# Kernel tuning notes

Measured on AMD Instinct MI355X. Metric: run time of the kernel, lower is better.

## Reference

```python
import jax, jax.numpy as jnp
import numpy as np
from jax import lax

N = 100000
IN_C, HID, OUT_C = 512, 256, 128
K_STEPS = 10
ALPHA = 0.1
RES_ALPHA = 1.0
LN_EPS = 1e-5


def layer_norm(h, g, b):
    mu = jnp.mean(h, axis=-1, keepdims=True)
    var = jnp.mean(jnp.square(h - mu), axis=-1, keepdims=True)
    return (h - mu) * lax.rsqrt(var + LN_EPS) * g + b


def appnp(h, src, dst):
    # add self loops
    loop = jnp.arange(N, dtype=src.dtype)
    s = jnp.concatenate([src, loop])
    d = jnp.concatenate([dst, loop])
    ew = jnp.ones(s.shape[0], h.dtype)
    deg = jax.ops.segment_sum(ew, d, num_segments=N)
    dis = jnp.where(deg > 0, lax.rsqrt(jnp.maximum(deg, 1e-12)), 0.0)
    norm = dis[s] * ew * dis[d]  # [E+N]
    h0 = h
    def step(carry, _):
        msg = norm[:, None] * carry[s]                      # gather [E+N, C]
        agg = jax.ops.segment_sum(msg, d, num_segments=N)    # scatter-add
        return (1.0 - ALPHA) * agg + ALPHA * h0, None
    h, _ = lax.scan(step, h, None, length=K_STEPS)
    return h


def setup_inputs() -> dict:
    key = jax.random.key(0)
    ks = jax.random.split(key, 12)
    def lin(k, fan_in, fan_out):
        bound = 1.0 / np.sqrt(fan_in)
        kw, kb = jax.random.split(k)
        W = jax.random.uniform(kw, (fan_in, fan_out), jnp.float32, -bound, bound)
        b = jax.random.uniform(kb, (fan_out,), jnp.float32, -bound, bound)
        return W, b
    x = jax.random.normal(ks[0], (N, IN_C), jnp.float32)
    edge_index = jax.random.randint(ks[1], (2, 1600000), 0, N, jnp.int32)
    W_in, b_in = lin(ks[2], IN_C, HID)
    W1, b1 = lin(ks[3], HID, HID)
    W2, b2 = lin(ks[4], HID, HID)
    W_out, b_out = lin(ks[5], HID, OUT_C)
    g1 = jnp.ones(HID); be1 = jnp.zeros(HID)
    g2 = jnp.ones(HID); be2 = jnp.zeros(HID)
    return {"x": x, "edge_index": edge_index,
            "W_in": W_in, "b_in": b_in,
            "W1": W1, "b1": b1, "g1": g1, "be1": be1,
            "W2": W2, "b2": b2, "g2": g2, "be2": be2,
            "W_out": W_out, "b_out": b_out}


def reference(x, edge_index, W_in, b_in, W1, b1, g1, be1, W2, b2, g2, be2, W_out, b_out):
    # MLP with residual blocks (eval mode: no dropout)
    h = x @ W_in + b_in
    for (W, b, g, be) in ((W1, b1, g1, be1), (W2, b2, g2, be2)):
        identity = h
        h = layer_norm(h @ W + b, g, be)
        h = RES_ALPHA * h + (1.0 - RES_ALPHA) * identity
        h = jax.nn.relu(h)
    h = h @ W_out + b_out
    # APPNP propagation
    return appnp(h, edge_index[0], edge_index[1])
```

## Files before the change

kernel.cpp:

```cpp
#include <hip/hip_runtime.h>

typedef unsigned short u16;
typedef unsigned long long u64;
typedef __attribute__((ext_vector_type(8))) short bfrag;
typedef __attribute__((ext_vector_type(4))) float f32x4;

__device__ inline float b2f(u16 u) {
    union { unsigned int i; float f; } v; v.i = ((unsigned int)u) << 16; return v.f;
}
__device__ inline u16 f2b(float f) {
    union { float f; unsigned int u; } v; v.f = f;
    unsigned int r = v.u + 0x7fffu + ((v.u >> 16) & 1u);
    return (u16)(r >> 16);
}
__device__ inline float ldF(const void* p, size_t i, bool bf) {
    return bf ? b2f(((const u16*)p)[i]) : ((const float*)p)[i];
}
__device__ inline void gload_lds16(const void* g, void* l) {
    __builtin_amdgcn_global_load_lds((const __attribute__((address_space(1))) unsigned int*)g,
                                     (__attribute__((address_space(3))) unsigned int*)l, 16, 0, 0);
}

__global__ void detect_k(const unsigned int* __restrict__ g1w, int* flag) {
    if (blockIdx.x == 0 && threadIdx.x == 0)
        *flag = (g1w[0] == 0x3F803F80u) ? 1 : 0;
}

__global__ void wt_k(const void* __restrict__ W, u16* __restrict__ Wt, int K, int NC,
                     const int* __restrict__ flagp) {
    int i = blockIdx.x * 256 + threadIdx.x;
    if (i >= K * NC) return;
    int k = i / NC, nn = i - k * NC;
    u16 v = (*flagp) ? ((const u16*)W)[i] : f2b(((const float*)W)[i]);
    Wt[(size_t)nn * K + k] = v;
}

template<int K, bool OUT_BF16, bool A_DUAL>
__global__ __launch_bounds__(256) void gemm_bt(const void* __restrict__ Ain, const u16* __restrict__ Bt,
                                               const void* __restrict__ bias, void* __restrict__ C,
                                               int M, int NC, const int* __restrict__ flagp) {
    const int BM = 128, BN = 128, BK = 32;
    __shared__ u16 As[2][BM * BK];
    __shared__ u16 Bs[2][BN * BK];
    const bool bf = (*flagp != 0);
    int nt = NC / BN;

    int nwg = gridDim.x, bid = blockIdx.x;
    int qc = nwg >> 3, rc = nwg & 7;
    int xcd = bid & 7, off = bid >> 3;
    int swz = (xcd < rc ? xcd * (qc + 1) : rc * (qc + 1) + (xcd - rc) * qc) + off;
    int m0 = (swz / nt) * BM;
    int n0 = (swz % nt) * BN;

    int t = threadIdx.x;
    int lane = t & 63, wave = t >> 6;
    int wm = (wave >> 1) * 64, wn = (wave & 1) * 64;

    f32x4 acc[4][4];
#pragma unroll
    for (int i = 0; i < 4; i++)
#pragma unroll
        for (int j = 0; j < 4; j++) acc[i][j] = (f32x4){0.f, 0.f, 0.f, 0.f};

    auto stage = [&](int bufi, int kk) {
#pragma unroll
        for (int q = 0; q < 2; ++q) {
            int idx = q * 256 + t;
            int row = idx >> 2;
            int cb  = (idx & 3) * 16;
            int ra = m0 + row; ra = ra < M ? ra : M - 1;
            const char* gb = (const char*)Bt + ((size_t)(n0 + row) * K) * 2 + kk * 2 + cb;
            char* la = (char*)&As[bufi][0] + q * 4096 + wave * 1024;
            char* lb = (char*)&Bs[bufi][0] + q * 4096 + wave * 1024;
            if (!A_DUAL || bf) {
                const char* ga = (const char*)Ain + ((size_t)ra * K) * 2 + kk * 2 + cb;
                gload_lds16(ga, la);
            } else {
                const float* gaf = (const float*)Ain + (size_t)ra * K + kk + (cb >> 1);
                float4 f0 = *(const float4*)gaf;
                float4 f1 = *(const float4*)(gaf + 4);
                ushort4 o0, o1;
                o0.x = f2b(f0.x); o0.y = f2b(f0.y); o0.z = f2b(f0.z); o0.w = f2b(f0.w);
                o1.x = f2b(f1.x); o1.y = f2b(f1.y); o1.z = f2b(f1.z); o1.w = f2b(f1.w);
                *(ushort4*)(la + (size_t)lane * 16)     = o0;
                *(ushort4*)(la + (size_t)lane * 16 + 8) = o1;
            }
            gload_lds16(gb, lb);
        }
    };

    stage(0, 0);
    __syncthreads();
    int cur = 0;
    int r16 = lane & 15, q8 = (lane >> 4) * 8;
    for (int k0 = 0; k0 < K; k0 += BK) {
        if (k0 + BK < K) stage(cur ^ 1, k0 + BK);
        bfrag a[4], b[4];
#pragma unroll
        for (int i = 0; i < 4; i++) a[i] = *(const bfrag*)&As[cur][(wm + i * 16 + r16) * BK + q8];
#pragma unroll
        for (int j = 0; j < 4; j++) b[j] = *(const bfrag*)&Bs[cur][(wn + j * 16 + r16) * BK + q8];
#pragma unroll
        for (int i = 0; i < 4; i++)
#pragma unroll
            for (int j = 0; j < 4; j++)
                acc[i][j] = __builtin_amdgcn_mfma_f32_16x16x32_bf16(a[i], b[j], acc[i][j], 0, 0, 0);
        __syncthreads();
        cur ^= 1;
    }

    int q4 = (lane >> 4) * 4;
#pragma unroll
    for (int j = 0; j < 4; j++) {
        int cg = n0 + wn + j * 16 + r16;
        float bvv = ldF(bias, cg, bf);
#pragma unroll
        for (int i = 0; i < 4; i++) {
#pragma unroll
            for (int rr = 0; rr < 4; rr++) {
                int rg = m0 + wm + i * 16 + q4 + rr;
                if (rg < M) {
                    float v = acc[i][j][rr] + bvv;
                    if (OUT_BF16) ((u16*)C)[(size_t)rg * NC + cg] = f2b(v);
                    else          ((float*)C)[(size_t)rg * NC + cg] = v;
                }
            }
        }
    }
}

__global__ __launch_bounds__(256) void ln_relu_k(const u16* __restrict__ T, const void* __restrict__ g,
                                                 const void* __restrict__ be, u16* __restrict__ out,
                                                 int M, const int* __restrict__ flagp) {
    const bool bf = (*flagp != 0);
    int wave = threadIdx.x >> 6, lane = threadIdx.x & 63;
    int row = blockIdx.x * 4 + wave;
    if (row >= M) return;
    const ushort4 xq = *(const ushort4*)(T + (size_t)row * 256 + lane * 4);
    float x0 = b2f(xq.x), x1 = b2f(xq.y), x2 = b2f(xq.z), x3 = b2f(xq.w);
    float s = x0 + x1 + x2 + x3;
    for (int o = 32; o > 0; o >>= 1) s += __shfl_xor(s, o);
    float mu = s * (1.0f / 256.0f);
    float d0 = x0 - mu, d1 = x1 - mu, d2 = x2 - mu, d3 = x3 - mu;
    float q = d0 * d0 + d1 * d1 + d2 * d2 + d3 * d3;
    for (int o = 32; o > 0; o >>= 1) q += __shfl_xor(q, o);
    float rs = rsqrtf(q * (1.0f / 256.0f) + 1e-5f);
    int c0 = lane * 4;
    float y0 = fmaxf(d0 * rs * ldF(g, c0 + 0, bf) + ldF(be, c0 + 0, bf), 0.f);
    float y1 = fmaxf(d1 * rs * ldF(g, c0 + 1, bf) + ldF(be, c0 + 1, bf), 0.f);
    float y2 = fmaxf(d2 * rs * ldF(g, c0 + 2, bf) + ldF(be, c0 + 2, bf), 0.f);
    float y3 = fmaxf(d3 * rs * ldF(g, c0 + 3, bf) + ldF(be, c0 + 3, bf), 0.f);
    ushort4 o4; o4.x = f2b(y0); o4.y = f2b(y1); o4.z = f2b(y2); o4.w = f2b(y3);
    *(ushort4*)(out + (size_t)row * 256 + c0) = o4;
}

__global__ void deg_count(const int* __restrict__ dst, int* deg, int E) {
    int i = blockIdx.x * 256 + threadIdx.x;
    if (i < E) atomicAdd(&deg[dst[i]], 1);
}
__global__ void dis_k(const int* __restrict__ deg, float* dis, int n) {
    int i = blockIdx.x * 256 + threadIdx.x;
    if (i < n) dis[i] = rsqrtf((float)(deg[i] + 1));
}

__global__ void scan_block(const int* __restrict__ deg, int* rowptr, int* bsum, int n) {
    __shared__ int sh[256];
    int t = threadIdx.x, i = blockIdx.x * 256 + t;
    int v = (i < n) ? deg[i] + 1 : 0;
    sh[t] = v; __syncthreads();
    for (int o = 1; o < 256; o <<= 1) {
        int x = (t >= o) ? sh[t - o] : 0;
        __syncthreads();
        sh[t] += x;
        __syncthreads();
    }
    if (i < n) rowptr[i] = sh[t] - v;
    if (t == 255) bsum[blockIdx.x] = sh[t];
}
__global__ void scan_sums(int* bsum, int nb) {
    __shared__ int sh[512];
    int t = threadIdx.x;
    int v = (t < nb) ? bsum[t] : 0;
    sh[t] = v; __syncthreads();
    for (int o = 1; o < 512; o <<= 1) {
        int x = (t >= o) ? sh[t - o] : 0;
        __syncthreads();
        sh[t] += x;
        __syncthreads();
    }
    if (t < nb) bsum[t] = sh[t] - v;
}
__global__ void scan_add(int* rowptr, const int* __restrict__ bsum, int n, int total) {
    int i = blockIdx.x * 256 + threadIdx.x;
    if (i < n) rowptr[i] += bsum[blockIdx.x];
    if (i == 0) rowptr[n] = total;
}
__global__ void fill_k(const int* __restrict__ src, const int* __restrict__ dst,
                       const int* __restrict__ rowptr, int* cursor, const float* __restrict__ dis,
                       int2* __restrict__ epack, int E, int n) {
    int i = blockIdx.x * 256 + threadIdx.x;
    if (i >= E + n) return;
    int s, d;
    if (i < E) { s = src[i]; d = dst[i]; }
    else       { s = d = i - E; }
    int p = rowptr[d] + atomicAdd(&cursor[d], 1);
    float wv = dis[s] * dis[d];
    u64 e = ((u64)__float_as_uint(wv) << 32) | (unsigned int)s;
    __builtin_nontemporal_store(e, (u64*)&epack[p]);
}

__global__ __launch_bounds__(256) void prop_k(const u16* __restrict__ curb, const u16* __restrict__ h0b,
                                              const int* __restrict__ rowptr, const int2* __restrict__ epack,
                                              u16* __restrict__ outB, void* __restrict__ outD,
                                              const int* __restrict__ flagp, int n) {
    int wave = threadIdx.x >> 6, lane = threadIdx.x & 63;
    int node = blockIdx.x * 4 + wave;
    if (node >= n) return;
    int p0 = rowptr[node], p1 = rowptr[node + 1];
    float ax = 0.f, ay = 0.f;
    for (int p = p0; p < p1; p += 64) {
        int cnt = p1 - p; if (cnt > 64) cnt = 64;
        int sj = 0; float wj = 0.f;
        if (lane < cnt) {
            u64 e = __builtin_nontemporal_load((const u64*)(epack + p + lane));
            sj = (int)(unsigned int)e;
            wj = __uint_as_float((unsigned int)(e >> 32));
        }
        int j = 0;
        for (; j + 16 <= cnt; j += 16) {
            float ww[16]; unsigned int v[16];
#pragma unroll
            for (int u = 0; u < 16; ++u) {
                int ss = __shfl(sj, j + u);
                ww[u] = __shfl(wj, j + u);
                v[u] = *(const unsigned int*)(curb + (size_t)ss * 128 + 2 * lane);
            }
#pragma unroll
            for (int u = 0; u < 16; ++u) {
                ax = fmaf(ww[u], b2f((u16)(v[u] & 0xffffu)), ax);
                ay = fmaf(ww[u], b2f((u16)(v[u] >> 16)), ay);
            }
        }
        for (; j < cnt; j += 8) {
            float ww[8]; unsigned int v[8];
#pragma unroll
            for (int u = 0; u < 8; ++u) {
                int jj = j + u;
                bool ok = jj < cnt;
                if (!ok) jj = cnt - 1;
                int ss = __shfl(sj, jj);
                float w2 = __shfl(wj, jj);
                ww[u] = ok ? w2 : 0.f;
                v[u] = *(const unsigned int*)(curb + (size_t)ss * 128 + 2 * lane);
            }
#pragma unroll
            for (int u = 0; u < 8; ++u) {
                ax = fmaf(ww[u], b2f((u16)(v[u] & 0xffffu)), ax);
                ay = fmaf(ww[u], b2f((u16)(v[u] >> 16)), ay);
            }
        }
    }
    unsigned int hp = __builtin_nontemporal_load((const unsigned int*)h0b + (size_t)node * 64 + lane);
    float rx = 0.9f * ax + 0.1f * b2f((u16)(hp & 0xffffu));
    float ry = 0.9f * ay + 0.1f * b2f((u16)(hp >> 16));
    unsigned int pk = ((unsigned int)f2b(ry) << 16) | (unsigned int)f2b(rx);
    if (outB) {
        __builtin_nontemporal_store(pk, (unsigned int*)outB + (size_t)node * 64 + lane);
    } else if (*flagp) {
        __builtin_nontemporal_store(pk, (unsigned int*)outD + (size_t)node * 64 + lane);
    } else {
        u64 o = ((u64)__float_as_uint(ry) << 32) | __float_as_uint(rx);
        __builtin_nontemporal_store(o, (u64*)((float*)outD + (size_t)node * 128 + 2 * lane));
    }
}

extern "C" void kernel_launch(void* const* d_in, const int* in_sizes, int n_in,
                              void* d_out, int out_size, void* d_ws, size_t ws_size,
                              hipStream_t stream) {
    const int N = in_sizes[0] / 512;
    const int E = in_sizes[1] / 2;
    const void* x    = d_in[0];
    const int*  ei   = (const int*)d_in[1];
    const void* Win  = d_in[2];
    const void* bin  = d_in[3];
    const void* W1   = d_in[4];
    const void* b1   = d_in[5];
    const void* g1   = d_in[6];
    const void* be1  = d_in[7];
    const void* W2   = d_in[8];
    const void* b2   = d_in[9];
    const void* g2   = d_in[10];
    const void* be2  = d_in[11];
    const void* Wout = d_in[12];
    const void* bout = d_in[13];
    (void)n_in; (void)out_size; (void)ws_size;

    char* w = (char*)d_ws;
    auto alloc = [&](size_t b) { char* p = w; w += (b + 255) & ~(size_t)255; return p; };
    char*  buf0 = alloc((size_t)N * 512 * 2);
    char*  actAraw = alloc((size_t)N * 256 * 2);
    u16* WtIn  = (u16*)alloc((size_t)512 * 256 * 2);
    u16* Wt1   = (u16*)alloc((size_t)256 * 256 * 2);
    u16* Wt2   = (u16*)alloc((size_t)256 * 256 * 2);
    u16* WtOut = (u16*)alloc((size_t)256 * 128 * 2);
    int*   deg    = (int*)alloc((size_t)N * 4);
    float* dis    = (float*)alloc((size_t)N * 4);
    int*   rowptr = (int*)alloc((size_t)(N + 1) * 4);
    int*   cursor = (int*)alloc((size_t)N * 4);
    int*   bsum   = (int*)alloc(512 * 4);
    int*   flag   = (int*)alloc(256);
    u16*   Tb  = (u16*)buf0;
    u16*   h0b = (u16*)buf0;
    u16*   cA  = (u16*)(buf0 + (size_t)N * 128 * 2);
    u16*   cB  = (u16*)(buf0 + (size_t)N * 128 * 4);
    u16*   actA  = (u16*)actAraw;
    int2*  epack = (int2*)actAraw;

    detect_k<<<1, 64, 0, stream>>>((const unsigned int*)g1, flag);

    wt_k<<<(512 * 256 + 255) / 256, 256, 0, stream>>>(Win,  WtIn,  512, 256, flag);
    wt_k<<<(256 * 256 + 255) / 256, 256, 0, stream>>>(W1,   Wt1,   256, 256, flag);
    wt_k<<<(256 * 256 + 255) / 256, 256, 0, stream>>>(W2,   Wt2,   256, 256, flag);
    wt_k<<<(256 * 128 + 255) / 256, 256, 0, stream>>>(Wout, WtOut, 256, 128, flag);

    int mt = (N + 127) / 128;
    gemm_bt<512, true , true ><<<mt * 2, 256, 0, stream>>>(x,    WtIn,  bin,  actA, N, 256, flag);
    gemm_bt<256, true , false><<<mt * 2, 256, 0, stream>>>(actA, Wt1,   b1,   Tb,   N, 256, flag);
    ln_relu_k<<<(N + 3) / 4, 256, 0, stream>>>(Tb, g1, be1, actA, N, flag);
    gemm_bt<256, true , false><<<mt * 2, 256, 0, stream>>>(actA, Wt2,   b2,   Tb,   N, 256, flag);
    ln_relu_k<<<(N + 3) / 4, 256, 0, stream>>>(Tb, g2, be2, actA, N, flag);
    gemm_bt<256, true , false><<<mt * 1, 256, 0, stream>>>(actA, WtOut, bout, h0b,  N, 128, flag);

    hipMemsetAsync(deg, 0, (size_t)N * 4, stream);
    deg_count<<<(E + 255) / 256, 256, 0, stream>>>(ei + E, deg, E);
    dis_k    <<<(N + 255) / 256, 256, 0, stream>>>(deg, dis, N);
    int nb = (N + 255) / 256;
    scan_block<<<nb, 256, 0, stream>>>(deg, rowptr, bsum, N);
    scan_sums<<<1, 512, 0, stream>>>(bsum, nb);
    scan_add<<<nb, 256, 0, stream>>>(rowptr, bsum, N, E + N);
    hipMemsetAsync(cursor, 0, (size_t)N * 4, stream);
    fill_k<<<(E + N + 255) / 256, 256, 0, stream>>>(ei, ei + E, rowptr, cursor, dis, epack, E, N);

    const u16* cur = h0b;
    for (int it = 0; it < 10; ++it) {
        bool last = (it == 9);
        u16* o = (it & 1) ? cB : cA;
        prop_k<<<(N + 3) / 4, 256, 0, stream>>>(cur, h0b, rowptr, epack,
                                                last ? nullptr : o,
                                                last ? d_out : nullptr, flag, N);
        cur = o;
    }
}
```

Measured before the change: 1.451 ms.

## Overlap fp32 A loads with MFMA and stage GEMM epilogue through LDS

For the fp32-input GEMM, the A tile's global loads are now issued before the MFMAs and converted and written to LDS after them, so load latency overlaps compute instead of stalling the stage. The epilogue writes bf16 results into a swizzled LDS tile and then stores full 16-byte rows, replacing scattered 2-byte global stores. Shared memory is merged into one 32KB buffer reused for the output tile. The cost is extra registers for the prefetched floats and one more barrier per block.

```diff
diff --git a/kernel.cpp b/kernel.cpp
--- a/kernel.cpp
+++ b/kernel.cpp
@@ -35,13 +35,12 @@
     Wt[(size_t)nn * K + k] = v;
 }
 
-template<int K, bool OUT_BF16, bool A_DUAL>
+template<int K, bool A_DUAL>
 __global__ __launch_bounds__(256) void gemm_bt(const void* __restrict__ Ain, const u16* __restrict__ Bt,
-                                               const void* __restrict__ bias, void* __restrict__ C,
+                                               const void* __restrict__ bias, u16* __restrict__ C,
                                                int M, int NC, const int* __restrict__ flagp) {
     const int BM = 128, BN = 128, BK = 32;
-    __shared__ u16 As[2][BM * BK];
-    __shared__ u16 Bs[2][BN * BK];
+    __shared__ u16 sh[16384];
     const bool bf = (*flagp != 0);
     int nt = NC / BN;
 
@@ -62,49 +61,71 @@
 #pragma unroll
         for (int j = 0; j < 4; j++) acc[i][j] = (f32x4){0.f, 0.f, 0.f, 0.f};
 
-    auto stage = [&](int bufi, int kk) {
+    char* shb = (char*)sh;
+    auto ldsA = [&](int bufi) { return shb + bufi * 8192; };
+    auto ldsB = [&](int bufi) { return shb + 16384 + bufi * 8192; };
+
+    auto stageAsync = [&](int bufi, int kk) {
 #pragma unroll
         for (int q = 0; q < 2; ++q) {
-            int idx = q * 256 + t;
-            int row = idx >> 2;
-            int cb  = (idx & 3) * 16;
+            int idx = q * 256 + t, row = idx >> 2, cb = (idx & 3) * 16;
             int ra = m0 + row; ra = ra < M ? ra : M - 1;
-            const char* gb = (const char*)Bt + ((size_t)(n0 + row) * K) * 2 + kk * 2 + cb;
-            char* la = (char*)&As[bufi][0] + q * 4096 + wave * 1024;
-            char* lb = (char*)&Bs[bufi][0] + q * 4096 + wave * 1024;
-            if (!A_DUAL || bf) {
-                const char* ga = (const char*)Ain + ((size_t)ra * K) * 2 + kk * 2 + cb;
-                gload_lds16(ga, la);
-            } else {
-                const float* gaf = (const float*)Ain + (size_t)ra * K + kk + (cb >> 1);
-                float4 f0 = *(const float4*)gaf;
-                float4 f1 = *(const float4*)(gaf + 4);
-                ushort4 o0, o1;
-                o0.x = f2b(f0.x); o0.y = f2b(f0.y); o0.z = f2b(f0.z); o0.w = f2b(f0.w);
-                o1.x = f2b(f1.x); o1.y = f2b(f1.y); o1.z = f2b(f1.z); o1.w = f2b(f1.w);
-                *(ushort4*)(la + (size_t)lane * 16)     = o0;
-                *(ushort4*)(la + (size_t)lane * 16 + 8) = o1;
-            }
-            gload_lds16(gb, lb);
+            gload_lds16((const char*)Bt + ((size_t)(n0 + row) * K + kk) * 2 + cb,
+                        ldsB(bufi) + q * 4096 + wave * 1024);
+            if (!A_DUAL || bf)
+                gload_lds16((const char*)Ain + ((size_t)ra * K + kk) * 2 + cb,
+                            ldsA(bufi) + q * 4096 + wave * 1024);
         }
     };
-
-    stage(0, 0);
+    float4 fr[2][2];
+    auto loadA32 = [&](int kk) {
+#pragma unroll
+        for (int q = 0; q < 2; ++q) {
+            int idx = q * 256 + t, row = idx >> 2, cf = (idx & 3) * 8;
+            int ra = m0 + row; ra = ra < M ? ra : M - 1;
+            const float* g = (const float*)Ain + (size_t)ra * K + kk + cf;
+            fr[q][0] = *(const float4*)g;
+            fr[q][1] = *(const float4*)(g + 4);
+        }
+    };
+    auto writeA32 = [&](int bufi) {
+#pragma unroll
+        for (int q = 0; q < 2; ++q) {
+            ushort4 o0, o1;
+            o0.x = f2b(fr[q][0].x); o0.y = f2b(fr[q][0].y); o0.z = f2b(fr[q][0].z); o0.w = f2b(fr[q][0].w);
+            o1.x = f2b(fr[q][1].x); o1.y = f2b(fr[q][1].y); o1.z = f2b(fr[q][1].z); o1.w = f2b(fr[q][1].w);
+            char* la = ldsA(bufi) + q * 4096 + wave * 1024 + lane * 16;
+            *(ushort4*)la = o0;
+            *(ushort4*)(la + 8) = o1;
+        }
+    };
+
+    const bool a32 = A_DUAL && !bf;
+    if (a32) loadA32(0);
+    stageAsync(0, 0);
+    if (a32) writeA32(0);
     __syncthreads();
     int cur = 0;
     int r16 = lane & 15, q8 = (lane >> 4) * 8;
     for (int k0 = 0; k0 < K; k0 += BK) {
-        if (k0 + BK < K) stage(cur ^ 1, k0 + BK);
+        bool next = (k0 + BK < K);
+        if (next) {
+            if (a32) loadA32(k0 + BK);
+            stageAsync(cur ^ 1, k0 + BK);
+        }
+        const u16* Ac = (const u16*)ldsA(cur);
+        const u16* Bc = (const u16*)ldsB(cur);
         bfrag a[4], b[4];
 #pragma unroll
-        for (int i = 0; i < 4; i++) a[i] = *(const bfrag*)&As[cur][(wm + i * 16 + r16) * BK + q8];
-#pragma unroll
-        for (int j = 0; j < 4; j++) b[j] = *(const bfrag*)&Bs[cur][(wn + j * 16 + r16) * BK + q8];
+        for (int i = 0; i < 4; i++) a[i] = *(const bfrag*)&Ac[(wm + i * 16 + r16) * BK + q8];
+#pragma unroll
+        for (int j = 0; j < 4; j++) b[j] = *(const bfrag*)&Bc[(wn + j * 16 + r16) * BK + q8];
 #pragma unroll
         for (int i = 0; i < 4; i++)
 #pragma unroll
             for (int j = 0; j < 4; j++)
                 acc[i][j] = __builtin_amdgcn_mfma_f32_16x16x32_bf16(a[i], b[j], acc[i][j], 0, 0, 0);
+        if (next && a32) writeA32(cur ^ 1);
         __syncthreads();
         cur ^= 1;
     }
@@ -114,18 +135,28 @@
     for (int j = 0; j < 4; j++) {
         int cg = n0 + wn + j * 16 + r16;
         float bvv = ldF(bias, cg, bf);
+        int colb = (wn + j * 16 + r16) * 2;
 #pragma unroll
         for (int i = 0; i < 4; i++) {
 #pragma unroll
             for (int rr = 0; rr < 4; rr++) {
-                int rg = m0 + wm + i * 16 + q4 + rr;
-                if (rg < M) {
-                    float v = acc[i][j][rr] + bvv;
-                    if (OUT_BF16) ((u16*)C)[(size_t)rg * NC + cg] = f2b(v);
-                    else          ((float*)C)[(size_t)rg * NC + cg] = v;
-                }
-            }
-        }
+                int row = wm + i * 16 + q4 + rr;
+                int sw = colb ^ (((row >> 2) & 3) << 5);
+                *(u16*)(shb + row * 256 + sw) = f2b(acc[i][j][rr] + bvv);
+            }
+        }
+    }
+    __syncthreads();
+#pragma unroll
+    for (int pass = 0; pass < 8; ++pass) {
+        int u = pass * 256 + t;
+        int row = u >> 4;
+        int cb = (u & 15) * 16;
+        int sw = cb ^ (((row >> 2) & 3) << 5);
+        uint4 vv = *(const uint4*)(shb + row * 256 + sw);
+        int rg = m0 + row;
+        if (rg < M)
+            *(uint4*)((char*)C + ((size_t)rg * NC + n0) * 2 + cb) = vv;
     }
 }
 
@@ -324,12 +355,12 @@
     wt_k<<<(256 * 128 + 255) / 256, 256, 0, stream>>>(Wout, WtOut, 256, 128, flag);
 
     int mt = (N + 127) / 128;
-    gemm_bt<512, true , true ><<<mt * 2, 256, 0, stream>>>(x,    WtIn,  bin,  actA, N, 256, flag);
-    gemm_bt<256, true , false><<<mt * 2, 256, 0, stream>>>(actA, Wt1,   b1,   Tb,   N, 256, flag);
+    gemm_bt<512, true ><<<mt * 2, 256, 0, stream>>>(x,    WtIn,  bin,  actA, N, 256, flag);
+    gemm_bt<256, false><<<mt * 2, 256, 0, stream>>>(actA, Wt1,   b1,   Tb,   N, 256, flag);
     ln_relu_k<<<(N + 3) / 4, 256, 0, stream>>>(Tb, g1, be1, actA, N, flag);
-    gemm_bt<256, true , false><<<mt * 2, 256, 0, stream>>>(actA, Wt2,   b2,   Tb,   N, 256, flag);
+    gemm_bt<256, false><<<mt * 2, 256, 0, stream>>>(actA, Wt2,   b2,   Tb,   N, 256, flag);
     ln_relu_k<<<(N + 3) / 4, 256, 0, stream>>>(Tb, g2, be2, actA, N, flag);
-    gemm_bt<256, true , false><<<mt * 1, 256, 0, stream>>>(actA, WtOut, bout, h0b,  N, 128, flag);
+    gemm_bt<256, false><<<mt * 1, 256, 0, stream>>>(actA, WtOut, bout, h0b,  N, 128, flag);
 
     hipMemsetAsync(deg, 0, (size_t)N * 4, stream);
     deg_count<<<(E + 255) / 256, 256, 0, stream>>>(ei + E, deg, E);
```

Result: faster. 1.370 ms (-5.6%).
